# Optimization experiments

Hardware: AMD Instinct MI355X
Metric: run time of the kernel (lower is better)

## Reference

```python
import jax, jax.numpy as jnp
import numpy as np

NUM_HEADS = 32
NUM_KV_HEADS = 8
HEAD_DIM = 128
SCALE = 1.0 / np.sqrt(HEAD_DIM)
LENGTHS = np.array([1024, 768, 512, 896], dtype=np.int32)  # ragged prefill lengths


def setup_inputs() -> dict:
    key = jax.random.key(0)
    kq, kk, kv = jax.random.split(key, 3)
    total = int(LENGTHS.sum())  # 3200
    q = jax.random.normal(kq, (total, NUM_HEADS * HEAD_DIM), dtype=jnp.float32)
    k = jax.random.normal(kk, (total, NUM_KV_HEADS * HEAD_DIM), dtype=jnp.float32)
    v = jax.random.normal(kv, (total, NUM_KV_HEADS * HEAD_DIM), dtype=jnp.float32)
    cu = jnp.asarray(np.concatenate([[0], np.cumsum(LENGTHS)]), dtype=jnp.int32)
    return {"q": q, "k": k, "v": v, "cu_seqlens": cu, "max_seqlen": 1024}


def _varlen_attn(q, k, v, cu_seqlens, max_seqlen):
    # q: [T, H*D], k/v: [T, KVH*D]; cu_seqlens: [B+1]
    T = q.shape[0]
    B = cu_seqlens.shape[0] - 1
    S = max_seqlen
    q = q.reshape(T, NUM_HEADS, HEAD_DIM)
    k = k.reshape(T, NUM_KV_HEADS, HEAD_DIM)
    v = v.reshape(T, NUM_KV_HEADS, HEAD_DIM)

    tok = jnp.arange(T, dtype=jnp.int32)
    batch_id = jnp.searchsorted(cu_seqlens[1:], tok, side="right").astype(jnp.int32)
    pos = tok - cu_seqlens[batch_id]

    # pad to [B, S, h, d] (zeros beyond each sequence, like _varlen_to_padded)
    qp = jnp.zeros((B, S, NUM_HEADS, HEAD_DIM), q.dtype).at[batch_id, pos].set(q)
    kp = jnp.zeros((B, S, NUM_KV_HEADS, HEAD_DIM), k.dtype).at[batch_id, pos].set(k)
    vp = jnp.zeros((B, S, NUM_KV_HEADS, HEAD_DIM), v.dtype).at[batch_id, pos].set(v)

    # GQA: repeat_interleave kv heads to match q heads
    rep = NUM_HEADS // NUM_KV_HEADS
    kp = jnp.repeat(kp, rep, axis=2)
    vp = jnp.repeat(vp, rep, axis=2)

    scores = jnp.einsum("bqhd,bkhd->bhqk", qp, kp) * SCALE
    # causal mask only (matches torch SDPA is_causal=True on padded input;
    # with equal q/k lengths, padded keys are never attended by valid queries)
    qi = jnp.arange(S)[:, None]
    kj = jnp.arange(S)[None, :]
    scores = jnp.where(kj <= qi, scores, jnp.finfo(scores.dtype).min)
    attn = jax.nn.softmax(scores, axis=-1)
    outp = jnp.einsum("bhqk,bkhd->bqhd", attn, vp)

    # unpad back to varlen and flatten heads
    out = outp[batch_id, pos]  # [T, H, D]
    return out.reshape(T, NUM_HEADS * HEAD_DIM)


def reference(q, k, v, cu_seqlens, max_seqlen):
    return _varlen_attn(q, k, v, cu_seqlens, max_seqlen)
```

## Files before the change

### kernel.cpp

```cpp
#include <hip/hip_runtime.h>
#include <hip/hip_bf16.h>

#define NH 32
#define NKVH 8
#define HD 128
#define KT 64
#define QT 32

typedef __attribute__((ext_vector_type(8))) __bf16 bf16x8;
typedef __attribute__((ext_vector_type(4))) short s16x4;
typedef __attribute__((ext_vector_type(4))) float f32x4;
typedef __attribute__((ext_vector_type(2))) unsigned int u32x2;
typedef __attribute__((ext_vector_type(4))) unsigned int u32x4;

__device__ inline unsigned short f2bf(float f) {
    unsigned int u = __builtin_bit_cast(unsigned int, f);
    u += 0x7fffu + ((u >> 16) & 1u);
    return (unsigned short)(u >> 16);
}
__device__ inline unsigned int pk2(float lo, float hi) {
    return (unsigned int)f2bf(lo) | ((unsigned int)f2bf(hi) << 16);
}
__device__ inline f32x4 mfma16(bf16x8 a, bf16x8 b, f32x4 c) {
    return __builtin_amdgcn_mfma_f32_16x16x32_bf16(a, b, c, 0, 0, 0);
}
__device__ inline f32x4 mfma16k16(s16x4 a, s16x4 b, f32x4 c) {
#if __has_builtin(__builtin_amdgcn_mfma_f32_16x16x16bf16_1k)
    return __builtin_amdgcn_mfma_f32_16x16x16bf16_1k(a, b, c, 0, 0, 0);
#else
    f32x4 d = c;
    asm volatile("v_mfma_f32_16x16x16_bf16 %0, %1, %2, %0"
                 : "+v"(d) : "v"(a), "v"(b));
    return d;
#endif
}
__device__ inline void async16(unsigned short* lds, const unsigned short* g) {
    __builtin_amdgcn_global_load_lds(
        (const __attribute__((address_space(1))) unsigned int*)g,
        (__attribute__((address_space(3))) unsigned int*)lds, 16, 0, 0);
}

__global__ __launch_bounds__(256) void prep_k(const float* __restrict__ kg,
                                              unsigned short* __restrict__ kb,
                                              int nunits) {
    int u = blockIdx.x * 256 + threadIdx.x;
    if (u >= nunits) return;
    const float* p = kg + (size_t)u * 8;
    f32x4 a = *(const f32x4*)p;
    f32x4 b = *(const f32x4*)(p + 4);
    u32x4 r = {pk2(a[0], a[1]), pk2(a[2], a[3]), pk2(b[0], b[1]), pk2(b[2], b[3])};
    *(u32x4*)(kb + (size_t)u * 8) = r;
}

__global__ __launch_bounds__(256) void prep_vt(const float* __restrict__ vg,
                                               const int* __restrict__ cu,
                                               unsigned short* __restrict__ vt) {
    const int b = blockIdx.y, kvh = blockIdx.z;
    const int bstart = cu[b];
    const int L = cu[b + 1] - bstart;
    const int kv0 = blockIdx.x * 64;
    if (kv0 >= L) return;
    const int tid = threadIdx.x;
    const int wid = tid >> 6, lane = tid & 63;
    __shared__ __align__(16) unsigned short Vl[HD * 64];

    #pragma unroll
    for (int it = 0; it < 4; ++it) {
        int jp = wid * 8 + (lane >> 3);
        int c4 = (lane & 7) + it * 8;
        int j0 = jp * 2;
        int jj0 = kv0 + j0;
        f32x4 va = f32x4{0.f, 0.f, 0.f, 0.f}, vb = f32x4{0.f, 0.f, 0.f, 0.f};
        if (jj0 < L)     va = *(const f32x4*)&vg[(size_t)(bstart + jj0) * (NKVH * HD) + kvh * HD + c4 * 4];
        if (jj0 + 1 < L) vb = *(const f32x4*)&vg[(size_t)(bstart + jj0 + 1) * (NKVH * HD) + kvh * HD + c4 * 4];
        #pragma unroll
        for (int i = 0; i < 4; ++i) {
            int d = c4 * 4 + i;
            int idx = (d * 64 + j0) ^ ((d & 7) << 3);
            *(unsigned int*)&Vl[idx] = pk2(va[i], vb[i]);
        }
    }
    __syncthreads();

    const size_t vtb = (size_t)bstart * (NKVH * HD) + (size_t)kvh * HD * L;
    #pragma unroll
    for (int it = 0; it < 8; ++it) {
        int u = tid + it * 256;
        int d = u >> 4, c = u & 15;
        int j0 = c * 4;
        if (kv0 + j0 >= L) continue;
        int idx = d * 64 + (j0 ^ ((d & 7) << 3));
        u32x2 w = *(const u32x2*)&Vl[idx];
        *(u32x2*)&vt[vtb + (size_t)d * L + kv0 + j0] = w;
    }
}

__global__ __launch_bounds__(256, 2) void fa11(const float* __restrict__ qg,
                                               const unsigned short* __restrict__ kb,
                                               const unsigned short* __restrict__ vt,
                                               const int* __restrict__ cu,
                                               float* __restrict__ outg,
                                               int* __restrict__ ctr, int B) {
    const int tid = threadIdx.x;
    const int wid = tid >> 6, lane = tid & 63;
    const int lg = lane >> 4, lr = lane & 15;

    __shared__ __align__(16) unsigned short Klds[2][KT * HD];
    __shared__ __align__(16) unsigned short Vlds[2][HD * KT];
    __shared__ int s_item;

    int totalF = 0;
    {
        int prev = cu[0];
        #pragma unroll 1
        for (int bb = 0; bb < B; ++bb) {
            int nxt = cu[bb + 1];
            totalF += (nxt - prev + QT - 1) / QT;
            prev = nxt;
        }
    }
    const int totalItems = totalF * NKVH;
    const float scv = 0.08838834764831843f * 1.4426950408889634f;

    for (;;) {
        if (tid == 0) s_item = atomicAdd(ctr, 1);
        __syncthreads();
        const int item = s_item;
        if (item >= totalItems) return;

        const int kvh = item / totalF;
        const int f = item - kvh * totalF;
        int rem = f, bstart = 0, L = 0, nqf = 0, found = 0;
        int prev = cu[0];
        #pragma unroll 1
        for (int bb = 0; bb < B; ++bb) {
            int nxt = cu[bb + 1];
            int len = nxt - prev;
            int nq = (len + QT - 1) / QT;
            if (!found) {
                if (rem < nq) { bstart = prev; L = len; nqf = nq; found = 1; }
                else rem -= nq;
            }
            prev = nxt;
        }
        const int qt = nqf - 1 - rem;
        const int q0 = qt * QT;
        const int h = kvh * 4 + wid;

        bf16x8 qf0[4], qf1[4];
        #pragma unroll
        for (int kk = 0; kk < 4; ++kk) {
            int row0 = q0 + lr;
            int tok0 = bstart + (row0 < L ? row0 : L - 1);
            const float* p = &qg[(size_t)tok0 * (NH * HD) + h * HD + kk * 32 + lg * 8];
            f32x4 a = *(const f32x4*)p;
            f32x4 bq = *(const f32x4*)(p + 4);
            u32x4 r = {pk2(a[0] * scv, a[1] * scv), pk2(a[2] * scv, a[3] * scv),
                       pk2(bq[0] * scv, bq[1] * scv), pk2(bq[2] * scv, bq[3] * scv)};
            qf0[kk] = __builtin_bit_cast(bf16x8, r);
        }
        #pragma unroll
        for (int kk = 0; kk < 4; ++kk) {
            int row1 = q0 + 16 + lr;
            int tok1 = bstart + (row1 < L ? row1 : L - 1);
            const float* p = &qg[(size_t)tok1 * (NH * HD) + h * HD + kk * 32 + lg * 8];
            f32x4 a = *(const f32x4*)p;
            f32x4 bq = *(const f32x4*)(p + 4);
            u32x4 r = {pk2(a[0] * scv, a[1] * scv), pk2(a[2] * scv, a[3] * scv),
                       pk2(bq[0] * scv, bq[1] * scv), pk2(bq[2] * scv, bq[3] * scv)};
            qf1[kk] = __builtin_bit_cast(bf16x8, r);
        }

        f32x4 acc0[8], acc1[8];
        #pragma unroll
        for (int i = 0; i < 8; ++i) {
            acc0[i] = f32x4{0.f, 0.f, 0.f, 0.f};
            acc1[i] = f32x4{0.f, 0.f, 0.f, 0.f};
        }
        float lsum0 = 0.f, lsum1 = 0.f;

        const int ntiles = (q0 + QT + KT - 1) / KT;
        const unsigned short* kbase = kb + (size_t)bstart * (NKVH * HD) + kvh * HD;
        const unsigned short* vbase = vt + (size_t)bstart * (NKVH * HD) + (size_t)kvh * HD * L;

        auto STAGE = [&](int buf, int kv0) {
            unsigned short* Kd = Klds[buf];
            unsigned short* Vd = Vlds[buf];
            #pragma unroll
            for (int i = 0; i < 4; ++i) {
                int U = i * 256 + tid;
                int j = U >> 4, u = U & 15;
                int up = (u & 8) | ((u ^ j) & 7);
                int jj = kv0 + j; if (jj >= L) jj = L - 1;
                async16(Kd + (size_t)U * 8, kbase + (size_t)jj * (NKVH * HD) + up * 8);
            }
            #pragma unroll
            for (int i = 0; i < 4; ++i) {
                int U = i * 256 + tid;
                int d = U >> 3, u = U & 7;
                int up = u ^ (d & 7);
                int col = kv0 + up * 8;
                if (col > L - 8) col = L - 8;
                async16(Vd + (size_t)U * 8, vbase + (size_t)d * L + col);
            }
        };

        STAGE(0, 0);
        __syncthreads();

        for (int kt = 0; kt < ntiles; ++kt) {
            const int kv0 = kt * KT;
            const int buf = kt & 1;
            if (kt + 1 < ntiles) STAGE(buf ^ 1, kv0 + KT);

            const unsigned short* Kc = Klds[buf];
            const unsigned short* Vc = Vlds[buf];

            const int shi_raw = ((q0 + QT - 1 - kv0) >> 4) + 1;
            const int s_hi = shi_raw < 4 ? shi_raw : 4;
            const bool needmask = (kv0 + KT - 1) > q0;
            const int qpos0 = q0 + lr;
            const int qpos1 = q0 + 16 + lr;

            f32x4 st0[4], st1[4];
            __builtin_amdgcn_s_setprio(1);
            #pragma unroll
            for (int s = 0; s < 4; ++s) {
                if (s < s_hi) {
                    f32x4 a0 = f32x4{0.f, 0.f, 0.f, 0.f};
                    f32x4 a1 = f32x4{0.f, 0.f, 0.f, 0.f};
                    int row = s * 16 + lr;
                    #pragma unroll
                    for (int kk = 0; kk < 4; ++kk) {
                        int un = kk * 4 + lg;
                        int cs = ((un & 8) | ((un ^ row) & 7)) * 8;
                        bf16x8 kf = *(const bf16x8*)&Kc[row * HD + cs];
                        a0 = mfma16(kf, qf0[kk], a0);
                        a1 = mfma16(kf, qf1[kk], a1);
                    }
                    st0[s] = a0;
                    st1[s] = a1;
                }
            }
            __builtin_amdgcn_s_setprio(0);

            #pragma unroll
            for (int s = 0; s < 4; ++s) {
                if (s < s_hi) {
                    #pragma unroll
                    for (int r = 0; r < 4; ++r) {
                        int j = kv0 + s * 16 + lg * 4 + r;
                        float p0 = __builtin_amdgcn_exp2f(st0[s][r]);
                        float p1 = __builtin_amdgcn_exp2f(st1[s][r]);
                        p0 = (needmask && j > qpos0) ? 0.f : p0;
                        p1 = (needmask && j > qpos1) ? 0.f : p1;
                        st0[s][r] = p0;
                        st1[s][r] = p1;
                        lsum0 += p0;
                        lsum1 += p1;
                    }
                }
            }

            #pragma unroll
            for (int s = 0; s < 4; ++s) {
                if (s < s_hi) {
                    u32x2 pp0 = {pk2(st0[s][0], st0[s][1]), pk2(st0[s][2], st0[s][3])};
                    u32x2 pp1 = {pk2(st1[s][0], st1[s][1]), pk2(st1[s][2], st1[s][3])};
                    s16x4 pb0 = __builtin_bit_cast(s16x4, pp0);
                    s16x4 pb1 = __builtin_bit_cast(s16x4, pp1);
                    __builtin_amdgcn_s_setprio(1);
                    #pragma unroll
                    for (int dsb = 0; dsb < 8; ++dsb) {
                        int vrow = dsb * 16 + lr;
                        int c0 = (s * 16 + lg * 4) ^ ((vrow & 7) << 3);
                        s16x4 vf = *(const s16x4*)&Vc[vrow * 64 + c0];
                        acc0[dsb] = mfma16k16(vf, pb0, acc0[dsb]);
                        acc1[dsb] = mfma16k16(vf, pb1, acc1[dsb]);
                    }
                    __builtin_amdgcn_s_setprio(0);
                }
            }
            __syncthreads();
        }

        {
            float l = lsum0;
            l += __shfl_xor(l, 16);
            l += __shfl_xor(l, 32);
            int q = q0 + lr;
            if (q < L) {
                float inv = 1.0f / l;
                size_t base = (size_t)(bstart + q) * (NH * HD) + h * HD;
                #pragma unroll
                for (int dsb = 0; dsb < 8; ++dsb) {
                    f32x4 o = acc0[dsb] * inv;
                    *(f32x4*)&outg[base + dsb * 16 + lg * 4] = o;
                }
            }
        }
        {
            float l = lsum1;
            l += __shfl_xor(l, 16);
            l += __shfl_xor(l, 32);
            int q = q0 + 16 + lr;
            if (q < L) {
                float inv = 1.0f / l;
                size_t base = (size_t)(bstart + q) * (NH * HD) + h * HD;
                #pragma unroll
                for (int dsb = 0; dsb < 8; ++dsb) {
                    f32x4 o = acc1[dsb] * inv;
                    *(f32x4*)&outg[base + dsb * 16 + lg * 4] = o;
                }
            }
        }
    }
}

extern "C" void kernel_launch(void* const* d_in, const int* in_sizes, int n_in,
                              void* d_out, int out_size, void* d_ws, size_t ws_size,
                              hipStream_t stream) {
    const float* q = (const float*)d_in[0];
    const float* k = (const float*)d_in[1];
    const float* v = (const float*)d_in[2];
    const int* cu  = (const int*)d_in[3];
    int T = in_sizes[0] / (NH * HD);
    int B = in_sizes[3] - 1;

    unsigned short* kb = (unsigned short*)d_ws;
    unsigned short* vt = kb + (size_t)T * (NKVH * HD);
    int* ctr = (int*)(vt + (size_t)T * (NKVH * HD));

    hipMemsetAsync(ctr, 0, sizeof(int), stream);

    int nunits = T * (NKVH * HD) / 8;
    prep_k<<<(nunits + 255) / 256, 256, 0, stream>>>(k, kb, nunits);
    dim3 gvt((T + 63) / 64, B, NKVH);
    prep_vt<<<gvt, 256, 0, stream>>>(v, cu, vt);

    fa11<<<dim3(512), dim3(256), 0, stream>>>(q, kb, vt, cu, (float*)d_out, ctr, B);
}
```

Baseline: 97.20 us.

## Single-buffer K/V LDS with split staging, fuse prep kernels, double grid

Merges the K conversion and the V transpose into one prep kernel, which saves a launch. Attention now keeps a single LDS buffer each for K and V. K for the next tile is staged right after QK^T, and V after PV, so the copies overlap with softmax and the other matmul. Halving LDS use should allow more resident blocks, and the persistent grid grows to 1024 blocks. The softmax loop is split into masked and unmasked versions. The cost is extra barriers per tile and less prefetch lead time.

```diff
diff --git a/kernel.cpp b/kernel.cpp
--- a/kernel.cpp
+++ b/kernel.cpp
@@ -40,20 +40,10 @@
         (__attribute__((address_space(3))) unsigned int*)lds, 16, 0, 0);
 }
 
-__global__ __launch_bounds__(256) void prep_k(const float* __restrict__ kg,
-                                              unsigned short* __restrict__ kb,
-                                              int nunits) {
-    int u = blockIdx.x * 256 + threadIdx.x;
-    if (u >= nunits) return;
-    const float* p = kg + (size_t)u * 8;
-    f32x4 a = *(const f32x4*)p;
-    f32x4 b = *(const f32x4*)(p + 4);
-    u32x4 r = {pk2(a[0], a[1]), pk2(a[2], a[3]), pk2(b[0], b[1]), pk2(b[2], b[3])};
-    *(u32x4*)(kb + (size_t)u * 8) = r;
-}
-
-__global__ __launch_bounds__(256) void prep_vt(const float* __restrict__ vg,
+__global__ __launch_bounds__(256) void prep_kv(const float* __restrict__ kg,
+                                               const float* __restrict__ vg,
                                                const int* __restrict__ cu,
+                                               unsigned short* __restrict__ kb,
                                                unsigned short* __restrict__ vt) {
     const int b = blockIdx.y, kvh = blockIdx.z;
     const int bstart = cu[b];
@@ -80,6 +70,20 @@
             *(unsigned int*)&Vl[idx] = pk2(va[i], vb[i]);
         }
     }
+
+    #pragma unroll
+    for (int it = 0; it < 4; ++it) {
+        int u = tid + it * 256;
+        int j = u >> 4, c8 = u & 15;
+        int jj = kv0 + j;
+        if (jj < L) {
+            const float* p = &kg[(size_t)(bstart + jj) * (NKVH * HD) + kvh * HD + c8 * 8];
+            f32x4 a = *(const f32x4*)p;
+            f32x4 bq = *(const f32x4*)(p + 4);
+            u32x4 r = {pk2(a[0], a[1]), pk2(a[2], a[3]), pk2(bq[0], bq[1]), pk2(bq[2], bq[3])};
+            *(u32x4*)&kb[(size_t)(bstart + jj) * (NKVH * HD) + kvh * HD + c8 * 8] = r;
+        }
+    }
     __syncthreads();
 
     const size_t vtb = (size_t)bstart * (NKVH * HD) + (size_t)kvh * HD * L;
@@ -95,7 +99,7 @@
     }
 }
 
-__global__ __launch_bounds__(256, 2) void fa11(const float* __restrict__ qg,
+__global__ __launch_bounds__(256, 2) void fa13(const float* __restrict__ qg,
                                                const unsigned short* __restrict__ kb,
                                                const unsigned short* __restrict__ vt,
                                                const int* __restrict__ cu,
@@ -105,8 +109,8 @@
     const int wid = tid >> 6, lane = tid & 63;
     const int lg = lane >> 4, lr = lane & 15;
 
-    __shared__ __align__(16) unsigned short Klds[2][KT * HD];
-    __shared__ __align__(16) unsigned short Vlds[2][HD * KT];
+    __shared__ __align__(16) unsigned short Klds[KT * HD];
+    __shared__ __align__(16) unsigned short Vlds[HD * KT];
     __shared__ int s_item;
 
     int totalF = 0;
@@ -147,6 +151,35 @@
         const int q0 = qt * QT;
         const int h = kvh * 4 + wid;
 
+        const int ntiles = (q0 + QT + KT - 1) / KT;
+        const unsigned short* kbase = kb + (size_t)bstart * (NKVH * HD) + kvh * HD;
+        const unsigned short* vbase = vt + (size_t)bstart * (NKVH * HD) + (size_t)kvh * HD * L;
+
+        auto STAGE_K = [&](int kv0) {
+            #pragma unroll
+            for (int i = 0; i < 4; ++i) {
+                int U = i * 256 + tid;
+                int j = U >> 4, u = U & 15;
+                int up = (u & 8) | ((u ^ j) & 7);
+                int jj = kv0 + j; if (jj >= L) jj = L - 1;
+                async16(Klds + (size_t)U * 8, kbase + (size_t)jj * (NKVH * HD) + up * 8);
+            }
+        };
+        auto STAGE_V = [&](int kv0) {
+            #pragma unroll
+            for (int i = 0; i < 4; ++i) {
+                int U = i * 256 + tid;
+                int d = U >> 3, u = U & 7;
+                int up = u ^ (d & 7);
+                int col = kv0 + up * 8;
+                if (col > L - 8) col = L - 8;
+                async16(Vlds + (size_t)U * 8, vbase + (size_t)d * L + col);
+            }
+        };
+
+        STAGE_K(0);
+        STAGE_V(0);
+
         bf16x8 qf0[4], qf1[4];
         #pragma unroll
         for (int kk = 0; kk < 4; ++kk) {
@@ -179,42 +212,11 @@
         }
         float lsum0 = 0.f, lsum1 = 0.f;
 
-        const int ntiles = (q0 + QT + KT - 1) / KT;
-        const unsigned short* kbase = kb + (size_t)bstart * (NKVH * HD) + kvh * HD;
-        const unsigned short* vbase = vt + (size_t)bstart * (NKVH * HD) + (size_t)kvh * HD * L;
-
-        auto STAGE = [&](int buf, int kv0) {
-            unsigned short* Kd = Klds[buf];
-            unsigned short* Vd = Vlds[buf];
-            #pragma unroll
-            for (int i = 0; i < 4; ++i) {
-                int U = i * 256 + tid;
-                int j = U >> 4, u = U & 15;
-                int up = (u & 8) | ((u ^ j) & 7);
-                int jj = kv0 + j; if (jj >= L) jj = L - 1;
-                async16(Kd + (size_t)U * 8, kbase + (size_t)jj * (NKVH * HD) + up * 8);
-            }
-            #pragma unroll
-            for (int i = 0; i < 4; ++i) {
-                int U = i * 256 + tid;
-                int d = U >> 3, u = U & 7;
-                int up = u ^ (d & 7);
-                int col = kv0 + up * 8;
-                if (col > L - 8) col = L - 8;
-                async16(Vd + (size_t)U * 8, vbase + (size_t)d * L + col);
-            }
-        };
-
-        STAGE(0, 0);
         __syncthreads();
 
         for (int kt = 0; kt < ntiles; ++kt) {
             const int kv0 = kt * KT;
-            const int buf = kt & 1;
-            if (kt + 1 < ntiles) STAGE(buf ^ 1, kv0 + KT);
-
-            const unsigned short* Kc = Klds[buf];
-            const unsigned short* Vc = Vlds[buf];
+            const bool more = (kt + 1 < ntiles);
 
             const int shi_raw = ((q0 + QT - 1 - kv0) >> 4) + 1;
             const int s_hi = shi_raw < 4 ? shi_raw : 4;
@@ -234,7 +236,7 @@
                     for (int kk = 0; kk < 4; ++kk) {
                         int un = kk * 4 + lg;
                         int cs = ((un & 8) | ((un ^ row) & 7)) * 8;
-                        bf16x8 kf = *(const bf16x8*)&Kc[row * HD + cs];
+                        bf16x8 kf = *(const bf16x8*)&Klds[row * HD + cs];
                         a0 = mfma16(kf, qf0[kk], a0);
                         a1 = mfma16(kf, qf1[kk], a1);
                     }
@@ -244,20 +246,36 @@
             }
             __builtin_amdgcn_s_setprio(0);
 
-            #pragma unroll
-            for (int s = 0; s < 4; ++s) {
-                if (s < s_hi) {
-                    #pragma unroll
-                    for (int r = 0; r < 4; ++r) {
-                        int j = kv0 + s * 16 + lg * 4 + r;
-                        float p0 = __builtin_amdgcn_exp2f(st0[s][r]);
-                        float p1 = __builtin_amdgcn_exp2f(st1[s][r]);
-                        p0 = (needmask && j > qpos0) ? 0.f : p0;
-                        p1 = (needmask && j > qpos1) ? 0.f : p1;
-                        st0[s][r] = p0;
-                        st1[s][r] = p1;
-                        lsum0 += p0;
-                        lsum1 += p1;
+            __syncthreads();
+            if (more) STAGE_K(kv0 + KT);
+
+            if (needmask) {
+                #pragma unroll
+                for (int s = 0; s < 4; ++s) {
+                    if (s < s_hi) {
+                        #pragma unroll
+                        for (int r = 0; r < 4; ++r) {
+                            int j = kv0 + s * 16 + lg * 4 + r;
+                            float p0 = __builtin_amdgcn_exp2f(st0[s][r]);
+                            float p1 = __builtin_amdgcn_exp2f(st1[s][r]);
+                            p0 = (j > qpos0) ? 0.f : p0;
+                            p1 = (j > qpos1) ? 0.f : p1;
+                            st0[s][r] = p0; st1[s][r] = p1;
+                            lsum0 += p0;   lsum1 += p1;
+                        }
+                    }
+                }
+            } else {
+                #pragma unroll
+                for (int s = 0; s < 4; ++s) {
+                    if (s < s_hi) {
+                        #pragma unroll
+                        for (int r = 0; r < 4; ++r) {
+                            float p0 = __builtin_amdgcn_exp2f(st0[s][r]);
+                            float p1 = __builtin_amdgcn_exp2f(st1[s][r]);
+                            st0[s][r] = p0; st1[s][r] = p1;
+                            lsum0 += p0;   lsum1 += p1;
+                        }
                     }
                 }
             }
@@ -274,14 +292,18 @@
                     for (int dsb = 0; dsb < 8; ++dsb) {
                         int vrow = dsb * 16 + lr;
                         int c0 = (s * 16 + lg * 4) ^ ((vrow & 7) << 3);
-                        s16x4 vf = *(const s16x4*)&Vc[vrow * 64 + c0];
+                        s16x4 vf = *(const s16x4*)&Vlds[vrow * 64 + c0];
                         acc0[dsb] = mfma16k16(vf, pb0, acc0[dsb]);
                         acc1[dsb] = mfma16k16(vf, pb1, acc1[dsb]);
                     }
                     __builtin_amdgcn_s_setprio(0);
                 }
             }
-            __syncthreads();
+
+            if (more) {
+                __syncthreads();
+                STAGE_V(kv0 + KT);
+            }
         }
 
         {
@@ -333,10 +355,8 @@
 
     hipMemsetAsync(ctr, 0, sizeof(int), stream);
 
-    int nunits = T * (NKVH * HD) / 8;
-    prep_k<<<(nunits + 255) / 256, 256, 0, stream>>>(k, kb, nunits);
-    dim3 gvt((T + 63) / 64, B, NKVH);
-    prep_vt<<<gvt, 256, 0, stream>>>(v, cu, vt);
-
-    fa11<<<dim3(512), dim3(256), 0, stream>>>(q, kb, vt, cu, (float*)d_out, ctr, B);
-}
+    dim3 gkv((T + 63) / 64, B, NKVH);
+    prep_kv<<<gkv, 256, 0, stream>>>(k, v, cu, kb, vt);
+
+    fa13<<<dim3(1024), dim3(256), 0, stream>>>(q, kb, vt, cu, (float*)d_out, ctr, B);
+}
```

Result: slower. 220.0 us (+126.4%).
